# Optimization experiments

Hardware: AMD Instinct MI355X
Metric: run time of the kernel (lower is better)

The kernel has to match this reference:

```python
import jax, jax.numpy as jnp
import numpy as np

B, T = 32, 4096
DIM_VECT, DIM_ATTN = 512, 256
DIM_ATTN_BID = 2 * DIM_ATTN  # flag_bid=True


def setup_inputs() -> dict:
    key = jax.random.key(0)
    k1, k2, k3, k4, k5, k6 = jax.random.split(key, 6)
    s = lambda fan_in: 1.0 / np.sqrt(fan_in)
    return {
        "vector": jax.random.normal(k1, (B, DIM_VECT), dtype=jnp.float32),
        "matrix": jax.random.normal(k2, (B, T, DIM_ATTN_BID), dtype=jnp.float32),
        "input_lengths": jax.random.randint(k3, (B,), 1, T + 1, dtype=jnp.int64),
        # nn.Linear weights are [out_features, in_features]
        "W_vec": jax.random.uniform(k4, (DIM_ATTN, DIM_VECT), jnp.float32, -s(DIM_VECT), s(DIM_VECT)),
        "W_mat": jax.random.uniform(k5, (DIM_ATTN, DIM_ATTN_BID), jnp.float32, -s(DIM_ATTN_BID), s(DIM_ATTN_BID)),
        "W_attn": jax.random.uniform(k6, (1, DIM_ATTN), jnp.float32, -s(DIM_ATTN), s(DIM_ATTN)),
    }


def reference(vector, matrix, input_lengths, W_vec, W_mat, W_attn):
    # vector: [B, Dv], matrix: [B, T, Dm], lengths: [B]
    t1 = jnp.einsum("bd,ad->ba", vector, W_vec)          # [B, A]
    t2 = jnp.einsum("btd,ad->bta", matrix, W_mat)        # [B, T, A]
    t3 = jax.nn.relu(t1[:, None, :] + t2)                # [B, T, A]
    logits = jnp.einsum("bta,oa->bt", t3, W_attn)        # [B, T] (o == 1 squeezed)
    # original subtracts the GLOBAL max over the whole logits tensor
    unnorm = jnp.exp(logits - logits.max())              # [B, T]
    mask = jnp.arange(matrix.shape[1])[None, :] < input_lengths[:, None]
    masked = unnorm * mask.astype(unnorm.dtype)
    attentions = masked / masked.sum(axis=1, keepdims=True)
    representations = jnp.einsum("btd,bt->bd", matrix, attentions)
    return representations, attentions
```

## Files before the change

kernel.cpp:

```cpp
#include <hip/hip_runtime.h>
#include <hip/hip_bf16.h>
#include <math.h>

#define B_SZ 32
#define T_SZ 4096
#define DV   512
#define DA   256
#define DK   512

typedef __attribute__((ext_vector_type(8))) __bf16 bf16x8;
typedef __attribute__((ext_vector_type(4))) __bf16 bf16x4;
typedef __attribute__((ext_vector_type(4))) float  f32x4;

__device__ inline int get_len(const int* __restrict__ p, int b) {
    return (p[1] == 0) ? p[2 * b] : p[b];
}

__global__ void setup_kernel(const float* __restrict__ wmat, __bf16* __restrict__ wmat_bf,
                             const float* __restrict__ vector, const float* __restrict__ wvec,
                             float* __restrict__ t1, float* __restrict__ rep) {
    int blk = blockIdx.x, tid = threadIdx.x;
    if (blk < 128) {
        int i = (blk * 256 + tid) * 4;
        float4 v = *(const float4*)(wmat + i);
        bf16x4 o;
        o[0] = (__bf16)v.x; o[1] = (__bf16)v.y; o[2] = (__bf16)v.z; o[3] = (__bf16)v.w;
        *(bf16x4*)(wmat_bf + i) = o;
        return;
    }
    int b = blk - 128;
    __shared__ float sv[DV];
    sv[tid]       = vector[b * DV + tid];
    sv[tid + 256] = vector[b * DV + tid + 256];
    rep[b * DV + tid]       = 0.f;
    rep[b * DV + tid + 256] = 0.f;
    __syncthreads();
    const float4* w  = (const float4*)(wvec + (size_t)tid * DV);
    const float4* s4 = (const float4*)sv;
    float acc = 0.f;
#pragma unroll 8
    for (int k = 0; k < DV / 4; k++) {
        float4 wv = w[k]; float4 xv = s4[k];
        acc += wv.x * xv.x + wv.y * xv.y + wv.z * xv.z + wv.w * xv.w;
    }
    t1[b * DA + tid] = acc;
}

#define TM  64
#define LDA 72

__global__ __launch_bounds__(256) void logits_kernel(
    const float* __restrict__ matrix, const __bf16* __restrict__ wmat,
    const float* __restrict__ t1, const float* __restrict__ wattn,
    const int* __restrict__ lens, float* __restrict__ logits) {
    int b  = blockIdx.y;
    int t0 = blockIdx.x * TM;
    int len = get_len(lens, b);
    if (t0 >= len) return;

    __shared__ __bf16 sA[2][TM][LDA];
    __shared__ float s_t1[DA];
    __shared__ float s_wa[DA];
    __shared__ float s_logit[TM];

    int tid = threadIdx.x;
    s_t1[tid] = t1[b * DA + tid];
    s_wa[tid] = wattn[tid];
    if (tid < TM) s_logit[tid] = 0.f;

    int wave = tid >> 6, lane = tid & 63;
    int col  = lane & 15;
    int koff = (lane >> 4) * 8;

    int srow = tid >> 4;
    int soff = (tid & 15) * 4;

    const float* Abase = matrix + ((size_t)b * T_SZ + t0) * DK;
    const __bf16* Bp[4];
#pragma unroll
    for (int nt = 0; nt < 4; nt++)
        Bp[nt] = wmat + (size_t)(wave * 64 + nt * 16 + col) * DK + koff;

    f32x4 acc[4][4];
    f32x4 zero = {0.f, 0.f, 0.f, 0.f};
#pragma unroll
    for (int i = 0; i < 4; i++)
#pragma unroll
        for (int j = 0; j < 4; j++) acc[i][j] = zero;

    {
#pragma unroll
        for (int r = 0; r < 4; r++) {
            float4 v = *(const float4*)(Abase + (size_t)(srow + r * 16) * DK + soff);
            bf16x4 o;
            o[0] = (__bf16)v.x; o[1] = (__bf16)v.y; o[2] = (__bf16)v.z; o[3] = (__bf16)v.w;
            *(bf16x4*)&sA[0][srow + r * 16][soff] = o;
        }
    }
    uint4 pb[8];
#pragma unroll
    for (int s = 0; s < 2; s++)
#pragma unroll
        for (int nt = 0; nt < 4; nt++)
            pb[s * 4 + nt] = *(const uint4*)(Bp[nt] + s * 32);

    __syncthreads();

    for (int ks = 0; ks < 8; ks++) {
        int buf = ks & 1;
        float4 na[4];
        uint4  nb[8];
        if (ks < 7) {
            int k1 = (ks + 1) * 64;
#pragma unroll
            for (int r = 0; r < 4; r++)
                na[r] = *(const float4*)(Abase + (size_t)(srow + r * 16) * DK + k1 + soff);
#pragma unroll
            for (int s = 0; s < 2; s++)
#pragma unroll
                for (int nt = 0; nt < 4; nt++)
                    nb[s * 4 + nt] = *(const uint4*)(Bp[nt] + k1 + s * 32);
        }
        bf16x8 af[2][4];
#pragma unroll
        for (int s = 0; s < 2; s++)
#pragma unroll
            for (int mt = 0; mt < 4; mt++)
                af[s][mt] = *(const bf16x8*)&sA[buf][mt * 16 + col][s * 32 + koff];
#pragma unroll
        for (int s = 0; s < 2; s++)
#pragma unroll
            for (int mt = 0; mt < 4; mt++)
#pragma unroll
                for (int nt = 0; nt < 4; nt++)
                    acc[mt][nt] = __builtin_amdgcn_mfma_f32_16x16x32_bf16(
                        af[s][mt], *(bf16x8*)&pb[s * 4 + nt], acc[mt][nt], 0, 0, 0);
        if (ks < 7) {
#pragma unroll
            for (int r = 0; r < 4; r++) {
                bf16x4 o;
                o[0] = (__bf16)na[r].x; o[1] = (__bf16)na[r].y;
                o[2] = (__bf16)na[r].z; o[3] = (__bf16)na[r].w;
                *(bf16x4*)&sA[buf ^ 1][srow + r * 16][soff] = o;
            }
#pragma unroll
            for (int i = 0; i < 8; i++) pb[i] = nb[i];
        }
        __syncthreads();
    }

    int rg = lane >> 4;
#pragma unroll
    for (int mt = 0; mt < 4; mt++) {
#pragma unroll
        for (int r = 0; r < 4; r++) {
            float v = 0.f;
#pragma unroll
            for (int nt = 0; nt < 4; nt++) {
                int a = wave * 64 + nt * 16 + col;
                float x = acc[mt][nt][r] + s_t1[a];
                v += s_wa[a] * fmaxf(x, 0.f);
            }
#pragma unroll
            for (int off = 1; off < 16; off <<= 1) v += __shfl_xor(v, off, 64);
            if (col == 0) atomicAdd(&s_logit[mt * 16 + rg * 4 + r], v);
        }
    }
    __syncthreads();
    if (tid < TM) logits[(size_t)b * T_SZ + t0 + tid] = s_logit[tid];
}

__global__ __launch_bounds__(1024) void softmax_kernel(const int* __restrict__ lens,
                                                       float* __restrict__ attn) {
    int b = blockIdx.x, tid = threadIdx.x;
    int len = get_len(lens, b);
    float* row = attn + (size_t)b * T_SZ;
    __shared__ float sred[16];

    float r[4];
#pragma unroll
    for (int i = 0; i < 4; i++) r[i] = row[tid + i * 1024];

    float m = -1e30f;
#pragma unroll
    for (int i = 0; i < 4; i++)
        if (tid + i * 1024 < len) m = fmaxf(m, r[i]);
#pragma unroll
    for (int off = 32; off; off >>= 1) m = fmaxf(m, __shfl_xor(m, off, 64));
    if ((tid & 63) == 0) sred[tid >> 6] = m;
    __syncthreads();
    m = sred[0];
#pragma unroll
    for (int i = 1; i < 16; i++) m = fmaxf(m, sred[i]);
    __syncthreads();

    float e[4];
    float s = 0.f;
#pragma unroll
    for (int i = 0; i < 4; i++) {
        e[i] = (tid + i * 1024 < len) ? __expf(r[i] - m) : 0.f;
        s += e[i];
    }
#pragma unroll
    for (int off = 32; off; off >>= 1) s += __shfl_xor(s, off, 64);
    if ((tid & 63) == 0) sred[tid >> 6] = s;
    __syncthreads();
    s = 0.f;
#pragma unroll
    for (int i = 0; i < 16; i++) s += sred[i];
    float inv = 1.f / s;

#pragma unroll
    for (int i = 0; i < 4; i++) row[tid + i * 1024] = e[i] * inv;
}

#define TC 128
__global__ void rep_kernel(const float* __restrict__ matrix, const float* __restrict__ attn,
                           const int* __restrict__ lens, float* __restrict__ rep) {
    int b = blockIdx.y, c = blockIdx.x, tid = threadIdx.x;
    int len = get_len(lens, b);
    int t0 = c * TC;
    if (t0 >= len) return;
    __shared__ float sa[TC];
    if (tid < TC) sa[tid] = attn[(size_t)b * T_SZ + t0 + tid];
    __syncthreads();
    int n = min(TC, len - t0);
    int half = tid >> 7;
    int l = tid & 127;
    int d = l * 4;
    int nh = (n + 1) >> 1;
    int tb = half ? nh : 0;
    int te = half ? n : nh;
    const float* M = matrix + ((size_t)b * T_SZ + t0) * DK;
    float a0 = 0.f, a1 = 0.f, a2 = 0.f, a3 = 0.f;
#pragma unroll 4
    for (int t = tb; t < te; t++) {
        float w = sa[t];
        float4 mv = *(const float4*)(M + (size_t)t * DK + d);
        a0 = fmaf(w, mv.x, a0); a1 = fmaf(w, mv.y, a1);
        a2 = fmaf(w, mv.z, a2); a3 = fmaf(w, mv.w, a3);
    }
    atomicAdd(&rep[b * DV + d],     a0);
    atomicAdd(&rep[b * DV + d + 1], a1);
    atomicAdd(&rep[b * DV + d + 2], a2);
    atomicAdd(&rep[b * DV + d + 3], a3);
}

extern "C" void kernel_launch(void* const* d_in, const int* in_sizes, int n_in,
                              void* d_out, int out_size, void* d_ws, size_t ws_size,
                              hipStream_t stream) {
    const float* vector = (const float*)d_in[0];
    const float* matrix = (const float*)d_in[1];
    const int*   lens   = (const int*)d_in[2];
    const float* wvec   = (const float*)d_in[3];
    const float* wmat   = (const float*)d_in[4];
    const float* wattn  = (const float*)d_in[5];

    float* rep  = (float*)d_out;
    float* attn = rep + B_SZ * DV;

    float*  t1      = (float*)d_ws;
    __bf16* wmat_bf = (__bf16*)((char*)d_ws + 32768);

    setup_kernel<<<dim3(160), 256, 0, stream>>>(wmat, wmat_bf, vector, wvec, t1, rep);
    logits_kernel<<<dim3(T_SZ / TM, B_SZ), 256, 0, stream>>>(matrix, wmat_bf, t1, wattn, lens, attn);
    softmax_kernel<<<dim3(B_SZ), 1024, 0, stream>>>(lens, attn);
    rep_kernel<<<dim3(T_SZ / TC, B_SZ), 256, 0, stream>>>(matrix, attn, lens, rep);
}
```

Measured before the change: 416.9 us.

## Fuse weighted sum into logits kernel via flash-style partial softmax combine

Each logits block now computes a local max and sum of exponentials for its 64 rows and immediately forms a partial weighted sum of its matrix tile, which is still resident in cache. A new combine kernel rescales these partials with the global max to produce the representation and normalised attentions. This replaces the separate softmax and rep kernels, so the second full pass over the large matrix and the global atomics go away. In exchange it writes and reads a per-block partial buffer and adds a tail to the logits kernel. It also subtracts the per-row max of valid entries rather than the reference's global max; this is algebraically equivalent after normalisation.

```diff
diff --git a/kernel.cpp b/kernel.cpp
--- a/kernel.cpp
+++ b/kernel.cpp
@@ -18,7 +18,7 @@
 
 __global__ void setup_kernel(const float* __restrict__ wmat, __bf16* __restrict__ wmat_bf,
                              const float* __restrict__ vector, const float* __restrict__ wvec,
-                             float* __restrict__ t1, float* __restrict__ rep) {
+                             float* __restrict__ t1) {
     int blk = blockIdx.x, tid = threadIdx.x;
     if (blk < 128) {
         int i = (blk * 256 + tid) * 4;
@@ -32,8 +32,6 @@
     __shared__ float sv[DV];
     sv[tid]       = vector[b * DV + tid];
     sv[tid + 256] = vector[b * DV + tid + 256];
-    rep[b * DV + tid]       = 0.f;
-    rep[b * DV + tid + 256] = 0.f;
     __syncthreads();
     const float4* w  = (const float4*)(wvec + (size_t)tid * DV);
     const float4* s4 = (const float4*)sv;
@@ -48,13 +46,16 @@
 
 #define TM  64
 #define LDA 72
+#define NBLK (T_SZ / TM)
 
 __global__ __launch_bounds__(256) void logits_kernel(
     const float* __restrict__ matrix, const __bf16* __restrict__ wmat,
     const float* __restrict__ t1, const float* __restrict__ wattn,
-    const int* __restrict__ lens, float* __restrict__ logits) {
+    const int* __restrict__ lens, float* __restrict__ logits,
+    float* __restrict__ P, float* __restrict__ ms) {
     int b  = blockIdx.y;
-    int t0 = blockIdx.x * TM;
+    int blk = blockIdx.x;
+    int t0 = blk * TM;
     int len = get_len(lens, b);
     if (t0 >= len) return;
 
@@ -62,6 +63,7 @@
     __shared__ float s_t1[DA];
     __shared__ float s_wa[DA];
     __shared__ float s_logit[TM];
+    __shared__ float sw[TM];
 
     int tid = threadIdx.x;
     s_t1[tid] = t1[b * DA + tid];
@@ -88,14 +90,12 @@
 #pragma unroll
         for (int j = 0; j < 4; j++) acc[i][j] = zero;
 
-    {
-#pragma unroll
-        for (int r = 0; r < 4; r++) {
-            float4 v = *(const float4*)(Abase + (size_t)(srow + r * 16) * DK + soff);
-            bf16x4 o;
-            o[0] = (__bf16)v.x; o[1] = (__bf16)v.y; o[2] = (__bf16)v.z; o[3] = (__bf16)v.w;
-            *(bf16x4*)&sA[0][srow + r * 16][soff] = o;
-        }
+#pragma unroll
+    for (int r = 0; r < 4; r++) {
+        float4 v = *(const float4*)(Abase + (size_t)(srow + r * 16) * DK + soff);
+        bf16x4 o;
+        o[0] = (__bf16)v.x; o[1] = (__bf16)v.y; o[2] = (__bf16)v.z; o[3] = (__bf16)v.w;
+        *(bf16x4*)&sA[0][srow + r * 16][soff] = o;
     }
     uint4 pb[8];
 #pragma unroll
@@ -167,83 +167,92 @@
         }
     }
     __syncthreads();
-    if (tid < TM) logits[(size_t)b * T_SZ + t0 + tid] = s_logit[tid];
-}
-
-__global__ __launch_bounds__(1024) void softmax_kernel(const int* __restrict__ lens,
-                                                       float* __restrict__ attn) {
+
+    if (tid < TM) {
+        float l = s_logit[tid];
+        bool valid = (t0 + tid) < len;
+        float m = valid ? l : -1e30f;
+#pragma unroll
+        for (int off = 32; off; off >>= 1) m = fmaxf(m, __shfl_xor(m, off, 64));
+        float w = valid ? __expf(l - m) : 0.f;
+        sw[tid] = w;
+        float s = w;
+#pragma unroll
+        for (int off = 32; off; off >>= 1) s += __shfl_xor(s, off, 64);
+        if (tid == 0) {
+            ms[(b * NBLK + blk) * 2]     = m;
+            ms[(b * NBLK + blk) * 2 + 1] = s;
+        }
+        logits[(size_t)b * T_SZ + t0 + tid] = l;
+    }
+    __syncthreads();
+
+    int d = 2 * tid;
+    int nv = min(TM, len - t0);
+    float p0 = 0.f, p1 = 0.f;
+#pragma unroll 4
+    for (int t = 0; t < nv; t++) {
+        float w = sw[t];
+        float2 mv = *(const float2*)(Abase + (size_t)t * DK + d);
+        p0 = fmaf(w, mv.x, p0);
+        p1 = fmaf(w, mv.y, p1);
+    }
+    float* Pb = P + ((size_t)(b * NBLK + blk)) * DV;
+    Pb[d]     = p0;
+    Pb[d + 1] = p1;
+}
+
+__global__ __launch_bounds__(1024) void combine_kernel(
+    const int* __restrict__ lens, const float* __restrict__ P,
+    const float* __restrict__ ms, float* __restrict__ rep,
+    float* __restrict__ attn) {
     int b = blockIdx.x, tid = threadIdx.x;
     int len = get_len(lens, b);
+    int nblk = (len + TM - 1) / TM;
+
+    __shared__ float sm[NBLK];
+    __shared__ float sscale[NBLK];
+    __shared__ float s_gm, s_gS;
+
+    if (tid < NBLK) {
+        if (tid < nblk) {
+            sm[tid]     = ms[(b * NBLK + tid) * 2];
+            sscale[tid] = ms[(b * NBLK + tid) * 2 + 1];
+        } else {
+            sm[tid] = -1e30f; sscale[tid] = 0.f;
+        }
+    }
+    __syncthreads();
+    if (tid < NBLK) {
+        float m = sm[tid];
+#pragma unroll
+        for (int off = 32; off; off >>= 1) m = fmaxf(m, __shfl_xor(m, off, 64));
+        float sc = (tid < nblk) ? __expf(sm[tid] - m) : 0.f;
+        float S = sc * sscale[tid];
+#pragma unroll
+        for (int off = 32; off; off >>= 1) S += __shfl_xor(S, off, 64);
+        sscale[tid] = sc;
+        if (tid == 0) { s_gm = m; s_gS = S; }
+    }
+    __syncthreads();
+    float m = s_gm;
+    float invS = 1.f / s_gS;
+
+    if (tid < DV) {
+        float acc = 0.f;
+        const float* Pb = P + (size_t)b * NBLK * DV + tid;
+        for (int blk = 0; blk < nblk; blk++)
+            acc += sscale[blk] * Pb[(size_t)blk * DV];
+        rep[b * DV + tid] = acc * invS;
+    }
+
     float* row = attn + (size_t)b * T_SZ;
-    __shared__ float sred[16];
-
-    float r[4];
-#pragma unroll
-    for (int i = 0; i < 4; i++) r[i] = row[tid + i * 1024];
-
-    float m = -1e30f;
-#pragma unroll
-    for (int i = 0; i < 4; i++)
-        if (tid + i * 1024 < len) m = fmaxf(m, r[i]);
-#pragma unroll
-    for (int off = 32; off; off >>= 1) m = fmaxf(m, __shfl_xor(m, off, 64));
-    if ((tid & 63) == 0) sred[tid >> 6] = m;
-    __syncthreads();
-    m = sred[0];
-#pragma unroll
-    for (int i = 1; i < 16; i++) m = fmaxf(m, sred[i]);
-    __syncthreads();
-
-    float e[4];
-    float s = 0.f;
-#pragma unroll
-    for (int i = 0; i < 4; i++) {
-        e[i] = (tid + i * 1024 < len) ? __expf(r[i] - m) : 0.f;
-        s += e[i];
-    }
-#pragma unroll
-    for (int off = 32; off; off >>= 1) s += __shfl_xor(s, off, 64);
-    if ((tid & 63) == 0) sred[tid >> 6] = s;
-    __syncthreads();
-    s = 0.f;
-#pragma unroll
-    for (int i = 0; i < 16; i++) s += sred[i];
-    float inv = 1.f / s;
-
-#pragma unroll
-    for (int i = 0; i < 4; i++) row[tid + i * 1024] = e[i] * inv;
-}
-
-#define TC 128
-__global__ void rep_kernel(const float* __restrict__ matrix, const float* __restrict__ attn,
-                           const int* __restrict__ lens, float* __restrict__ rep) {
-    int b = blockIdx.y, c = blockIdx.x, tid = threadIdx.x;
-    int len = get_len(lens, b);
-    int t0 = c * TC;
-    if (t0 >= len) return;
-    __shared__ float sa[TC];
-    if (tid < TC) sa[tid] = attn[(size_t)b * T_SZ + t0 + tid];
-    __syncthreads();
-    int n = min(TC, len - t0);
-    int half = tid >> 7;
-    int l = tid & 127;
-    int d = l * 4;
-    int nh = (n + 1) >> 1;
-    int tb = half ? nh : 0;
-    int te = half ? n : nh;
-    const float* M = matrix + ((size_t)b * T_SZ + t0) * DK;
-    float a0 = 0.f, a1 = 0.f, a2 = 0.f, a3 = 0.f;
-#pragma unroll 4
-    for (int t = tb; t < te; t++) {
-        float w = sa[t];
-        float4 mv = *(const float4*)(M + (size_t)t * DK + d);
-        a0 = fmaf(w, mv.x, a0); a1 = fmaf(w, mv.y, a1);
-        a2 = fmaf(w, mv.z, a2); a3 = fmaf(w, mv.w, a3);
-    }
-    atomicAdd(&rep[b * DV + d],     a0);
-    atomicAdd(&rep[b * DV + d + 1], a1);
-    atomicAdd(&rep[b * DV + d + 2], a2);
-    atomicAdd(&rep[b * DV + d + 3], a3);
+#pragma unroll
+    for (int i = 0; i < T_SZ / 1024; i++) {
+        int t = tid + i * 1024;
+        float l = row[t];
+        row[t] = (t < len) ? __expf(l - m) * invS : 0.f;
+    }
 }
 
 extern "C" void kernel_launch(void* const* d_in, const int* in_sizes, int n_in,
@@ -259,11 +268,14 @@
     float* rep  = (float*)d_out;
     float* attn = rep + B_SZ * DV;
 
-    float*  t1      = (float*)d_ws;
-    __bf16* wmat_bf = (__bf16*)((char*)d_ws + 32768);
-
-    setup_kernel<<<dim3(160), 256, 0, stream>>>(wmat, wmat_bf, vector, wvec, t1, rep);
-    logits_kernel<<<dim3(T_SZ / TM, B_SZ), 256, 0, stream>>>(matrix, wmat_bf, t1, wattn, lens, attn);
-    softmax_kernel<<<dim3(B_SZ), 1024, 0, stream>>>(lens, attn);
-    rep_kernel<<<dim3(T_SZ / TC, B_SZ), 256, 0, stream>>>(matrix, attn, lens, rep);
-}
+    char* ws = (char*)d_ws;
+    float*  t1      = (float*)ws;
+    __bf16* wmat_bf = (__bf16*)(ws + 32768);
+    float*  P       = (float*)(ws + 32768 + 262144);
+    float*  ms      = (float*)(ws + 32768 + 262144 + 4194304);
+
+    setup_kernel<<<dim3(160), 256, 0, stream>>>(wmat, wmat_bf, vector, wvec, t1);
+    logits_kernel<<<dim3(NBLK, B_SZ), 256, 0, stream>>>(matrix, wmat_bf, t1, wattn,
+                                                        lens, attn, P, ms);
+    combine_kernel<<<dim3(B_SZ), 1024, 0, stream>>>(lens, P, ms, rep, attn);
+}
```

Result: faster. 407.9 us (-2.2%).
